# Performance work log

Measured on AMD Instinct MI355X. Metric: run time of the kernel, lower is better.

The kernel has to match this reference:

```python
import jax, jax.numpy as jnp
import numpy as np

T = 4096      # tokens (flattened batch*seq)
DIN = 2048    # input hidden dim
DQ = 2048     # q output dim
DKV = 2048    # per-head-group kv output dim (== DQ here, MHA)
NA = 4        # number of adapters (LoRA/delta models)
R = 16        # lora rank per q/k/v


def setup_inputs() -> dict:
    key = jax.random.key(0)
    ks = jax.random.split(key, 8)
    def rn(k, shape, scale):
        return jax.random.normal(k, shape, dtype=jnp.float32) * scale
    return {
        "x": rn(ks[0], (T, DIN), 1.0),
        "W_base": rn(ks[1], (DQ + 2 * DKV, DIN), DIN ** -0.5),
        "A_buffer_qkv": rn(ks[2], (NA, DIN, 3 * R), DIN ** -0.5),
        "B_buffer_q": rn(ks[3], (NA, R, DQ), R ** -0.5),
        "B_buffer_kv": rn(ks[4], (NA, R, 2 * DKV), R ** -0.5),
        "DeltaW_q": rn(ks[5], (NA, DIN, DQ), DIN ** -0.5),
        "DeltaW_kv": rn(ks[6], (NA, DIN, 2 * DKV), DIN ** -0.5),
        "weight_indices": jax.random.randint(ks[7], (T,), 0, NA, dtype=jnp.int32),
    }


def _ldmm(indices, x, A, B, D):
    """Per-token adapter-indexed (LoRA + dense delta) matmul.
    indices: [T] int, x: [T, din], A: [na, din, r], B: [na, r, dout], D: [na, din, dout].
    out[t] = (x[t] @ A[a]) @ B[a] + x[t] @ D[a]  with a = indices[t].
    Implemented as masked GEMMs over the small fixed adapter set.
    """
    na = A.shape[0]
    out = jnp.zeros((x.shape[0], B.shape[2]), dtype=x.dtype)
    for a in range(na):  # small fixed loop over adapters
        xa = jnp.where((indices == a)[:, None], x, jnp.zeros((), x.dtype))
        out = out + (xa @ A[a]) @ B[a] + xa @ D[a]
    return out


def reference(x, W_base, A_buffer_qkv, B_buffer_q, B_buffer_kv,
              DeltaW_q, DeltaW_kv, weight_indices):
    # base QKV projection (ColumnParallelLinear, no bias): [T, dq + 2*dkv]
    base = x @ W_base.T
    rank = A_buffer_qkv.shape[2] // 3
    b_dim_q = B_buffer_q.shape[2]
    b_dim_kv = B_buffer_kv.shape[2] // 2
    d_dim_kv = DeltaW_kv.shape[2] // 2
    for i in range(3):  # q, k, v slices
        if i == 0:
            o = _ldmm(weight_indices, x,
                      A_buffer_qkv[:, :, :rank], B_buffer_q, DeltaW_q)
            base = base.at[:, :b_dim_q].add(o)
        else:
            o = _ldmm(weight_indices, x,
                      A_buffer_qkv[:, :, i * rank:(i + 1) * rank],
                      B_buffer_kv[:, :, (i - 1) * b_dim_kv:i * b_dim_kv],
                      DeltaW_kv[:, :, (i - 1) * d_dim_kv:i * d_dim_kv])
            base = base.at[:, i * b_dim_kv:(i + 1) * b_dim_kv].add(o)
    return base
```

## Files before the change

kernel.cpp:

```cpp
#include <hip/hip_runtime.h>
#include <stdint.h>

#define T_TOK 4096
#define DIN   2048
#define DQ    2048
#define DKV   2048
#define NOUT  (DQ + 2*DKV)
#define NA    4
#define RLORA 16
#define BM    256
#define BN    256
#define MPAD  (T_TOK + NA*BM)
#define MTILES (MPAD/BM)
#define KX    (DIN + 64)
#define NKT   (KX/32)
#define KSPLIT 16
#define NTBLK (NOUT/BN)
#define NWG   (MTILES*NTBLK)

typedef unsigned short u16;
typedef __attribute__((ext_vector_type(8))) short short8;
typedef __attribute__((ext_vector_type(8))) u16 u16x8;
typedef __attribute__((ext_vector_type(4))) float f32x4;

__device__ __forceinline__ u16 f2bf(float f) {
  uint32_t u = __float_as_uint(f);
  u = (u + 0x7FFFu + ((u >> 16) & 1u)) >> 16;
  return (u16)u;
}
__device__ __forceinline__ float bf2f(u16 u) {
  return __uint_as_float(((uint32_t)u) << 16);
}

typedef __attribute__((address_space(3))) void lds_void;
typedef __attribute__((address_space(1))) void glb_void;

__device__ __forceinline__ void gl_lds16(const void* g, void* l) {
  __builtin_amdgcn_global_load_lds((const glb_void*)(uintptr_t)g,
                                   (lds_void*)(uint32_t)(uintptr_t)l, 16, 0, 0);
}

__global__ void prep_kernel(const int* __restrict__ widx,
                            int* __restrict__ tok,
                            int* __restrict__ tileAdapter) {
  __shared__ int cnt[256][NA];
  __shared__ int total[NA];
  __shared__ int pad_off[NA];
  const int tid = threadIdx.x;
  const int CH = T_TOK / 256;
  const int base = tid * CH;
  int c[NA] = {0, 0, 0, 0};
  for (int i = 0; i < CH; i++) c[widx[base + i]]++;
  for (int a = 0; a < NA; a++) cnt[tid][a] = c[a];
  __syncthreads();
  if (tid < NA) {
    int s = 0;
    for (int i = 0; i < 256; i++) { int v = cnt[i][tid]; cnt[i][tid] = s; s += v; }
    total[tid] = s;
  }
  __syncthreads();
  if (tid == 0) {
    int off = 0;
    for (int a = 0; a < NA; a++) {
      pad_off[a] = off;
      int ntile = (total[a] + BM - 1) / BM;
      for (int tl = 0; tl < ntile; tl++) tileAdapter[off / BM + tl] = a;
      off += ntile * BM;
    }
    for (int tl = off / BM; tl < MTILES; tl++) tileAdapter[tl] = -1;
  }
  __syncthreads();
  for (int i = tid; i < MPAD; i += 256) tok[i] = -1;
  __syncthreads();
  int myoff[NA];
  for (int a = 0; a < NA; a++) myoff[a] = pad_off[a] + cnt[tid][a];
  for (int i = 0; i < CH; i++) {
    int a = widx[base + i];
    tok[myoff[a]++] = base + i;
  }
}

__global__ void gather_kernel(const float* __restrict__ x,
                              const int* __restrict__ tok,
                              u16* __restrict__ Xg) {
  const int row = blockIdx.x;
  const int t = tok[row];
  const int tid = threadIdx.x;
  u16x8* dst = (u16x8*)(Xg + (size_t)row * KX);
  if (t < 0) {
    u16x8 z = {0, 0, 0, 0, 0, 0, 0, 0};
    dst[tid] = z;
    return;
  }
  const f32x4* src = (const f32x4*)(x + (size_t)t * DIN);
  f32x4 v0 = src[tid * 2];
  f32x4 v1 = src[tid * 2 + 1];
  u16x8 o;
  o[0] = f2bf(v0[0]); o[1] = f2bf(v0[1]); o[2] = f2bf(v0[2]); o[3] = f2bf(v0[3]);
  o[4] = f2bf(v1[0]); o[5] = f2bf(v1[1]); o[6] = f2bf(v1[2]); o[7] = f2bf(v1[3]);
  dst[tid] = o;
}

__global__ __launch_bounds__(256) void xa_partial_kernel(
    const u16* __restrict__ Xg, const float* __restrict__ A_qkv,
    const int* __restrict__ tileAdapter, float* __restrict__ Ppart) {
  const int ks = blockIdx.y;
  const int ad = tileAdapter[blockIdx.x >> 1];
  const int a = ad < 0 ? 0 : ad;
  const int kb = ks * (DIN / KSPLIT);
  const int tid = threadIdx.x;
  const int rg = tid >> 2;
  const int jg = tid & 3;
  const int r0 = blockIdx.x * 128 + rg * 2;
  const int j0 = jg * 12;
  __shared__ float ldsA[64][56];
  float acc[2][12];
  #pragma unroll
  for (int r = 0; r < 2; r++)
    #pragma unroll
    for (int j = 0; j < 12; j++) acc[r][j] = 0.f;

  for (int kc = 0; kc < 2; kc++) {
    const int kbase = kb + kc * 64;
    for (int i = tid; i < 64 * 48; i += 256) {
      int kk = i / 48, j = i - kk * 48;
      ldsA[kk][j] = A_qkv[((size_t)a * DIN + kbase + kk) * (3 * RLORA) + j];
    }
    __syncthreads();
    u16x8 xr[2][8];
    #pragma unroll
    for (int r = 0; r < 2; r++)
      #pragma unroll
      for (int q = 0; q < 8; q++)
        xr[r][q] = *(const u16x8*)(Xg + (size_t)(r0 + r) * KX + kbase + q * 8);
    #pragma unroll
    for (int q = 0; q < 8; q++) {
      #pragma unroll
      for (int e = 0; e < 8; e++) {
        const int kk = q * 8 + e;
        f32x4 a0 = *(const f32x4*)&ldsA[kk][j0];
        f32x4 a1 = *(const f32x4*)&ldsA[kk][j0 + 4];
        f32x4 a2 = *(const f32x4*)&ldsA[kk][j0 + 8];
        float x0 = bf2f(xr[0][q][e]);
        float x1 = bf2f(xr[1][q][e]);
        #pragma unroll
        for (int c = 0; c < 4; c++) {
          acc[0][c]     += x0 * a0[c];  acc[1][c]     += x1 * a0[c];
          acc[0][4 + c] += x0 * a1[c];  acc[1][4 + c] += x1 * a1[c];
          acc[0][8 + c] += x0 * a2[c];  acc[1][8 + c] += x1 * a2[c];
        }
      }
    }
    __syncthreads();
  }
  #pragma unroll
  for (int r = 0; r < 2; r++)
    #pragma unroll
    for (int j = 0; j < 12; j++)
      Ppart[((size_t)ks * MPAD + r0 + r) * 48 + j0 + j] = acc[r][j];
}

__global__ void xa_reduce_kernel(const float* __restrict__ Ppart,
                                 u16* __restrict__ Xg) {
  const int gid = blockIdx.x * 256 + threadIdx.x;
  const int row = gid >> 6, j = gid & 63;
  float s = 0.f;
  if (j < 48) {
    #pragma unroll
    for (int sp = 0; sp < KSPLIT; sp++)
      s += Ppart[((size_t)sp * MPAD + row) * 48 + j];
  }
  Xg[(size_t)row * KX + DIN + j] = f2bf(s);
}

__global__ __launch_bounds__(256) void weff2_kernel(
    const float* __restrict__ W_base,
    const float* __restrict__ DW_q, const float* __restrict__ DW_kv,
    u16* __restrict__ Weff) {
  const int k0 = blockIdx.x * 64;
  const int n0 = blockIdx.y * 64;
  const int tid = threadIdx.x;
  const int k8 = (tid & 7) * 8;
  __shared__ float ldsD[64][65];

  f32x4 wb[2][2];
  #pragma unroll
  for (int h = 0; h < 2; h++) {
    const int nn = h * 32 + (tid >> 3);
    const float* p = W_base + (size_t)(n0 + nn) * DIN + k0 + k8;
    wb[h][0] = *(const f32x4*)p;
    wb[h][1] = *(const f32x4*)(p + 4);
  }

  const int ldD  = (n0 < DQ) ? DQ : 2 * DKV;
  const int ncol = (n0 < DQ) ? n0 : n0 - DQ;
  const float* Dbase = (n0 < DQ) ? (DW_q + ncol) : (DW_kv + ncol);
  const size_t Dstride = (n0 < DQ) ? (size_t)DIN * DQ : (size_t)DIN * (2 * DKV);

  const int lkk = tid >> 6;
  const int lnn = tid & 63;

  float v[16];
  {
    const float* Dp = Dbase;
    #pragma unroll
    for (int j = 0; j < 16; j++)
      v[j] = Dp[(size_t)(k0 + lkk + 4 * j) * ldD + lnn];
  }

  for (int a = 0; a < NA; a++) {
    #pragma unroll
    for (int j = 0; j < 16; j++) ldsD[lkk + 4 * j][lnn] = v[j];
    if (a < NA - 1) {
      const float* Dp = Dbase + (size_t)(a + 1) * Dstride;
      #pragma unroll
      for (int j = 0; j < 16; j++)
        v[j] = Dp[(size_t)(k0 + lkk + 4 * j) * ldD + lnn];
    }
    __syncthreads();
    #pragma unroll
    for (int h = 0; h < 2; h++) {
      const int nn = h * 32 + (tid >> 3);
      u16x8 o;
      #pragma unroll
      for (int j = 0; j < 8; j++)
        o[j] = f2bf(wb[h][j >> 2][j & 3] + ldsD[k8 + j][nn]);
      *(u16x8*)(Weff + ((size_t)a * NOUT + n0 + nn) * KX + k0 + k8) = o;
    }
    __syncthreads();
  }
}

__global__ void wslots_kernel(const float* __restrict__ B_q,
                              const float* __restrict__ B_kv,
                              u16* __restrict__ Weff) {
  const int a = blockIdx.y;
  const int n = blockIdx.x * 256 + threadIdx.x;
  const int seg = n >> 11;
  u16 vals[64];
  #pragma unroll
  for (int j = 0; j < 64; j++) vals[j] = 0;
  if (seg == 0) {
    const float* Bp = B_q + ((size_t)a * RLORA) * DQ + n;
    #pragma unroll
    for (int r = 0; r < RLORA; r++) vals[r] = f2bf(Bp[(size_t)r * DQ]);
  } else if (seg == 1) {
    const float* Bp = B_kv + ((size_t)a * RLORA) * (2 * DKV) + (n - DQ);
    #pragma unroll
    for (int r = 0; r < RLORA; r++) vals[RLORA + r] = f2bf(Bp[(size_t)r * (2 * DKV)]);
  } else {
    const float* Bp = B_kv + ((size_t)a * RLORA) * (2 * DKV) + (n - DQ);
    #pragma unroll
    for (int r = 0; r < RLORA; r++) vals[2 * RLORA + r] = f2bf(Bp[(size_t)r * (2 * DKV)]);
  }
  u16* dst = Weff + ((size_t)a * NOUT + n) * KX + DIN;
  #pragma unroll
  for (int v = 0; v < 8; v++) *(u16x8*)(dst + v * 8) = *(u16x8*)(vals + v * 8);
}

#define BAR      asm volatile("s_barrier" ::: "memory")
#define WAITV(n) asm volatile("s_waitcnt vmcnt(" #n ")" ::: "memory")

#define RD_A4(b, mlo) { \
  _Pragma("unroll") for (int q = 0; q < 4; ++q) { \
    const char* rp = ldsc + (b)*16384 + (wm*128 + ((mlo)+q)*16)*64; \
    af[(mlo)+q] = *(const short8*)(rp + laneoff); } }

#define RD_B4(b) { \
  _Pragma("unroll") for (int q = 0; q < 4; ++q) { \
    const char* rp = ldsc + 65536 + (b)*16384 + (wn*64 + q*16)*64; \
    bfr[q] = *(const short8*)(rp + laneoff); } }

#define ST_U01(b, t) { \
  gl_lds16(gAsrc + (size_t)(t)*32, ldsu + (b)*8192 + stid); \
  gl_lds16(gAsrc + (size_t)128*KX + (size_t)(t)*32, ldsu + (b)*8192 + 4096 + stid); }

#define ST_U23(b, t) { \
  gl_lds16(gBsrc + (size_t)(t)*32, ldsu + 32768 + (b)*8192 + stid); \
  gl_lds16(gBsrc + (size_t)128*KX + (size_t)(t)*32, ldsu + 32768 + (b)*8192 + 4096 + stid); }

#define MM4(mlo) { \
  __builtin_amdgcn_s_setprio(1); \
  _Pragma("unroll") for (int mi = 0; mi < 4; ++mi) \
  _Pragma("unroll") for (int ni = 0; ni < 4; ++ni) \
    acc[(mlo)+mi][ni] = __builtin_amdgcn_mfma_f32_16x16x32_bf16( \
        af[(mlo)+mi], bfr[ni], acc[(mlo)+mi][ni], 0, 0, 0); \
  __builtin_amdgcn_s_setprio(0); }

#define TILE(b, t, W) { \
  W; BAR; \
  RD_A4(b, 0); RD_B4(b); ST_U01(((b)+3)&3, (t)+3); \
  BAR; \
  MM4(0); \
  RD_A4(b, 4); ST_U23(((b)+3)&3, (t)+3); \
  BAR; \
  MM4(4); }

#define TILE_N(b, W) { \
  W; BAR; \
  RD_A4(b, 0); RD_B4(b); \
  BAR; \
  MM4(0); \
  RD_A4(b, 4); \
  BAR; \
  MM4(4); }

__global__ __launch_bounds__(512, 2) void gemm256_kernel(
    const u16* __restrict__ Xg, const u16* __restrict__ Weff,
    const int* __restrict__ tok, const int* __restrict__ tileAdapter,
    float* __restrict__ out) {
  __shared__ __align__(16) u16 Lds[65536];

  const int bid = blockIdx.x;
  const int lw = (bid & 7) * (NWG / 8) + (bid >> 3);
  const int pg  = lw / (2 * NTBLK);
  const int rem = lw % (2 * NTBLK);
  const int nt  = rem >> 1;
  const int mt  = pg * 2 + (rem & 1);
  const int a = tileAdapter[mt];
  if (a < 0) return;
  const int m0 = mt * BM, n0 = nt * BN;

  const int tid = threadIdx.x;
  const int l = tid & 63, w = tid >> 6;
  const int wm = w >> 2, wn = w & 3;
  const int fr = l & 15;
  const int laneoff = fr * 64 + ((((l >> 4) ^ ((fr >> 1) & 3))) << 4);

  const int srow = tid >> 2;
  const int scol = (((tid & 3) ^ ((tid >> 3) & 3))) * 8;
  const int stid = tid * 8;
  const u16* gAsrc = Xg + (size_t)(m0 + srow) * KX + scol;
  const u16* gBsrc = Weff + ((size_t)a * NOUT + n0 + srow) * KX + scol;

  u16* ldsu = &Lds[0];
  const char* ldsc = (const char*)ldsu;

  f32x4 acc[8][4];
  #pragma unroll
  for (int i = 0; i < 8; i++)
    #pragma unroll
    for (int j = 0; j < 4; j++) acc[i][j] = (f32x4){0.f, 0.f, 0.f, 0.f};

  short8 af[8], bfr[4];

  ST_U01(0, 0); ST_U23(0, 0);
  ST_U01(1, 1); ST_U23(1, 1);
  ST_U01(2, 2); ST_U23(2, 2);

  for (int p = 0; p < 15; ++p) {
    const int t4 = 4 * p;
    TILE(0, t4 + 0, WAITV(8));
    TILE(1, t4 + 1, WAITV(8));
    TILE(2, t4 + 2, WAITV(8));
    TILE(3, t4 + 3, WAITV(8));
  }
  TILE(0, 60, WAITV(8));
  TILE(1, 61, WAITV(8));
  TILE(2, 62, WAITV(8));
  TILE_N(3, WAITV(8));
  TILE_N(0, WAITV(4));
  TILE_N(1, WAITV(0));

  #pragma unroll
  for (int mi = 0; mi < 8; ++mi) {
    const int rb = m0 + wm * 128 + mi * 16 + ((l >> 4) << 2);
    int tt[4];
    #pragma unroll
    for (int reg = 0; reg < 4; ++reg) tt[reg] = tok[rb + reg];
    #pragma unroll
    for (int ni = 0; ni < 4; ++ni) {
      const int col = n0 + wn * 64 + ni * 16 + fr;
      #pragma unroll
      for (int reg = 0; reg < 4; ++reg)
        if (tt[reg] >= 0) out[(size_t)tt[reg] * NOUT + col] = acc[mi][ni][reg];
    }
  }
}

__global__ void fallback_kernel(const float* __restrict__ x,
                                const float* __restrict__ W_base,
                                const float* __restrict__ A_qkv,
                                const float* __restrict__ B_q,
                                const float* __restrict__ B_kv,
                                const float* __restrict__ DW_q,
                                const float* __restrict__ DW_kv,
                                const int* __restrict__ widx,
                                float* __restrict__ out) {
  const int t = blockIdx.x;
  const int n = blockIdx.y * 256 + threadIdx.x;
  const int a = widx[t];
  __shared__ float xs[DIN];
  __shared__ float ys[3 * RLORA];
  for (int k = threadIdx.x; k < DIN; k += 256) xs[k] = x[(size_t)t * DIN + k];
  __syncthreads();
  if (threadIdx.x < 3 * RLORA) {
    float s = 0.f;
    const float* Ap = A_qkv + (size_t)a * DIN * (3 * RLORA) + threadIdx.x;
    for (int k = 0; k < DIN; k++) s += xs[k] * Ap[(size_t)k * (3 * RLORA)];
    ys[threadIdx.x] = s;
  }
  __syncthreads();
  const float* dcol; int ldD, roff; const float* bcol; int ldB;
  if (n < DQ) {
    dcol = DW_q + (size_t)a * DIN * DQ + n; ldD = DQ; roff = 0;
    bcol = B_q + (size_t)a * RLORA * DQ + n; ldB = DQ;
  } else {
    dcol = DW_kv + (size_t)a * DIN * (2 * DKV) + (n - DQ); ldD = 2 * DKV;
    roff = (n < 2 * DQ) ? RLORA : 2 * RLORA;
    bcol = B_kv + (size_t)a * RLORA * (2 * DKV) + (n - DQ); ldB = 2 * DKV;
  }
  const float* wrow = W_base + (size_t)n * DIN;
  float acc = 0.f;
  for (int k = 0; k < DIN; k++) acc += xs[k] * (wrow[k] + dcol[(size_t)k * ldD]);
  for (int r = 0; r < RLORA; r++) acc += ys[roff + r] * bcol[(size_t)r * ldB];
  out[(size_t)t * NOUT + n] = acc;
}

extern "C" void kernel_launch(void* const* d_in, const int* in_sizes, int n_in,
                              void* d_out, int out_size, void* d_ws, size_t ws_size,
                              hipStream_t stream) {
  const float* x      = (const float*)d_in[0];
  const float* W_base = (const float*)d_in[1];
  const float* A_qkv  = (const float*)d_in[2];
  const float* B_q    = (const float*)d_in[3];
  const float* B_kv   = (const float*)d_in[4];
  const float* DW_q   = (const float*)d_in[5];
  const float* DW_kv  = (const float*)d_in[6];
  const int*   widx   = (const int*)d_in[7];
  float* out = (float*)d_out;

  const size_t WEFF_BYTES = (size_t)NA * NOUT * KX * sizeof(u16);
  const size_t XG_BYTES   = (size_t)MPAD * KX * sizeof(u16);
  const size_t TOK_BYTES  = (size_t)MPAD * sizeof(int);
  const size_t TILE_BYTES = (size_t)MTILES * sizeof(int);
  const size_t need = WEFF_BYTES + XG_BYTES + TOK_BYTES + TILE_BYTES;

  if (ws_size < need) {
    fallback_kernel<<<dim3(T_TOK, NOUT / 256), 256, 0, stream>>>(
        x, W_base, A_qkv, B_q, B_kv, DW_q, DW_kv, widx, out);
    return;
  }

  char* ws = (char*)d_ws;
  u16* Weff = (u16*)ws;
  u16* Xg   = (u16*)(ws + WEFF_BYTES);
  int* tok  = (int*)(ws + WEFF_BYTES + XG_BYTES);
  int* tileAdapter = tok + MPAD;
  float* Ppart = (float*)ws;

  prep_kernel<<<1, 256, 0, stream>>>(widx, tok, tileAdapter);
  gather_kernel<<<MPAD, 256, 0, stream>>>(x, tok, Xg);
  xa_partial_kernel<<<dim3(MPAD / 128, KSPLIT), 256, 0, stream>>>(
      Xg, A_qkv, tileAdapter, Ppart);
  xa_reduce_kernel<<<MPAD * 64 / 256, 256, 0, stream>>>(Ppart, Xg);
  weff2_kernel<<<dim3(DIN / 64, NOUT / 64), 256, 0, stream>>>(
      W_base, DW_q, DW_kv, Weff);
  wslots_kernel<<<dim3(NOUT / 256, NA), 256, 0, stream>>>(B_q, B_kv, Weff);
  gemm256_kernel<<<dim3(NWG), 512, 0, stream>>>(
      Xg, Weff, tok, tileAdapter, out);
}
```

Before: 257.4 us.

## Switch main GEMM to 4-wave workgroups with 128x128 per-wave tiles

The 256x256 GEMM tile moves from 8 waves (128x64 per wave) to 4 waves (128x128 per wave, 8x8 MFMA accumulators), launched with 256 threads and launch bounds of 1 block. The split LDS-read/MFMA phases with three barriers per k-step become one barrier per step, with all fragments read up front and then 64 MFMAs issued. The intent is more MFMA work per LDS fragment loaded and less barrier overhead. The cost is much higher register pressure (256 accumulator VGPRs), which risks spills, lower occupancy and less latency hiding.

```diff
diff --git a/kernel.cpp b/kernel.cpp
--- a/kernel.cpp
+++ b/kernel.cpp
@@ -261,51 +261,31 @@
 #define BAR      asm volatile("s_barrier" ::: "memory")
 #define WAITV(n) asm volatile("s_waitcnt vmcnt(" #n ")" ::: "memory")
 
-#define RD_A4(b, mlo) { \
-  _Pragma("unroll") for (int q = 0; q < 4; ++q) { \
-    const char* rp = ldsc + (b)*16384 + (wm*128 + ((mlo)+q)*16)*64; \
-    af[(mlo)+q] = *(const short8*)(rp + laneoff); } }
-
-#define RD_B4(b) { \
-  _Pragma("unroll") for (int q = 0; q < 4; ++q) { \
-    const char* rp = ldsc + 65536 + (b)*16384 + (wn*64 + q*16)*64; \
-    bfr[q] = *(const short8*)(rp + laneoff); } }
-
-#define ST_U01(b, t) { \
-  gl_lds16(gAsrc + (size_t)(t)*32, ldsu + (b)*8192 + stid); \
-  gl_lds16(gAsrc + (size_t)128*KX + (size_t)(t)*32, ldsu + (b)*8192 + 4096 + stid); }
-
-#define ST_U23(b, t) { \
-  gl_lds16(gBsrc + (size_t)(t)*32, ldsu + 32768 + (b)*8192 + stid); \
-  gl_lds16(gBsrc + (size_t)128*KX + (size_t)(t)*32, ldsu + 32768 + (b)*8192 + 4096 + stid); }
-
-#define MM4(mlo) { \
+#define ST(b, t) { \
+  _Pragma("unroll") for (int j = 0; j < 4; ++j) { \
+    gl_lds16(gAsrc + (size_t)(j * 64) * KX + (size_t)(t) * 32, \
+             ldsu + (b)*8192 + j*2048 + tid*8); \
+    gl_lds16(gBsrc + (size_t)(j * 64) * KX + (size_t)(t) * 32, \
+             ldsu + 32768 + (b)*8192 + j*2048 + tid*8); } }
+
+#define RD(b) { \
+  _Pragma("unroll") for (int q = 0; q < 8; ++q) \
+    af[q] = *(const short8*)(ldsc + (b)*16384 + (wm*128 + q*16)*64 + laneoff); \
+  _Pragma("unroll") for (int q = 0; q < 8; ++q) \
+    bf[q] = *(const short8*)(ldsc + 65536 + (b)*16384 + (wn*128 + q*16)*64 + laneoff); }
+
+#define MM64 { \
   __builtin_amdgcn_s_setprio(1); \
-  _Pragma("unroll") for (int mi = 0; mi < 4; ++mi) \
-  _Pragma("unroll") for (int ni = 0; ni < 4; ++ni) \
-    acc[(mlo)+mi][ni] = __builtin_amdgcn_mfma_f32_16x16x32_bf16( \
-        af[(mlo)+mi], bfr[ni], acc[(mlo)+mi][ni], 0, 0, 0); \
+  _Pragma("unroll") for (int q = 0; q < 8; ++q) \
+  _Pragma("unroll") for (int r = 0; r < 8; ++r) \
+    acc[q][r] = __builtin_amdgcn_mfma_f32_16x16x32_bf16( \
+        af[q], bf[r], acc[q][r], 0, 0, 0); \
   __builtin_amdgcn_s_setprio(0); }
 
-#define TILE(b, t, W) { \
-  W; BAR; \
-  RD_A4(b, 0); RD_B4(b); ST_U01(((b)+3)&3, (t)+3); \
-  BAR; \
-  MM4(0); \
-  RD_A4(b, 4); ST_U23(((b)+3)&3, (t)+3); \
-  BAR; \
-  MM4(4); }
-
-#define TILE_N(b, W) { \
-  W; BAR; \
-  RD_A4(b, 0); RD_B4(b); \
-  BAR; \
-  MM4(0); \
-  RD_A4(b, 4); \
-  BAR; \
-  MM4(4); }
-
-__global__ __launch_bounds__(512, 2) void gemm256_kernel(
+#define TILE_S(b, t) { WAITV(16); BAR; RD(b); ST(((b)+3)&3, (t)+3); MM64; }
+#define TILE_N(b, W) { W; BAR; RD(b); MM64; }
+
+__global__ __launch_bounds__(256, 1) void gemm4w_kernel(
     const u16* __restrict__ Xg, const u16* __restrict__ Weff,
     const int* __restrict__ tok, const int* __restrict__ tileAdapter,
     float* __restrict__ out) {
@@ -323,43 +303,40 @@
 
   const int tid = threadIdx.x;
   const int l = tid & 63, w = tid >> 6;
-  const int wm = w >> 2, wn = w & 3;
+  const int wm = w >> 1, wn = w & 1;
   const int fr = l & 15;
   const int laneoff = fr * 64 + ((((l >> 4) ^ ((fr >> 1) & 3))) << 4);
 
   const int srow = tid >> 2;
   const int scol = (((tid & 3) ^ ((tid >> 3) & 3))) * 8;
-  const int stid = tid * 8;
   const u16* gAsrc = Xg + (size_t)(m0 + srow) * KX + scol;
   const u16* gBsrc = Weff + ((size_t)a * NOUT + n0 + srow) * KX + scol;
 
   u16* ldsu = &Lds[0];
   const char* ldsc = (const char*)ldsu;
 
-  f32x4 acc[8][4];
+  f32x4 acc[8][8];
   #pragma unroll
   for (int i = 0; i < 8; i++)
     #pragma unroll
-    for (int j = 0; j < 4; j++) acc[i][j] = (f32x4){0.f, 0.f, 0.f, 0.f};
-
-  short8 af[8], bfr[4];
-
-  ST_U01(0, 0); ST_U23(0, 0);
-  ST_U01(1, 1); ST_U23(1, 1);
-  ST_U01(2, 2); ST_U23(2, 2);
+    for (int j = 0; j < 8; j++) acc[i][j] = (f32x4){0.f, 0.f, 0.f, 0.f};
+
+  short8 af[8], bf[8];
+
+  ST(0, 0); ST(1, 1); ST(2, 2);
 
   for (int p = 0; p < 15; ++p) {
     const int t4 = 4 * p;
-    TILE(0, t4 + 0, WAITV(8));
-    TILE(1, t4 + 1, WAITV(8));
-    TILE(2, t4 + 2, WAITV(8));
-    TILE(3, t4 + 3, WAITV(8));
-  }
-  TILE(0, 60, WAITV(8));
-  TILE(1, 61, WAITV(8));
-  TILE(2, 62, WAITV(8));
-  TILE_N(3, WAITV(8));
-  TILE_N(0, WAITV(4));
+    TILE_S(0, t4 + 0);
+    TILE_S(1, t4 + 1);
+    TILE_S(2, t4 + 2);
+    TILE_S(3, t4 + 3);
+  }
+  TILE_S(0, 60);
+  TILE_S(1, 61);
+  TILE_S(2, 62);
+  TILE_N(3, WAITV(16));
+  TILE_N(0, WAITV(8));
   TILE_N(1, WAITV(0));
 
   #pragma unroll
@@ -369,8 +346,8 @@
     #pragma unroll
     for (int reg = 0; reg < 4; ++reg) tt[reg] = tok[rb + reg];
     #pragma unroll
-    for (int ni = 0; ni < 4; ++ni) {
-      const int col = n0 + wn * 64 + ni * 16 + fr;
+    for (int ni = 0; ni < 8; ++ni) {
+      const int col = n0 + wn * 128 + ni * 16 + fr;
       #pragma unroll
       for (int reg = 0; reg < 4; ++reg)
         if (tt[reg] >= 0) out[(size_t)tt[reg] * NOUT + col] = acc[mi][ni][reg];
@@ -457,6 +434,6 @@
   weff2_kernel<<<dim3(DIN / 64, NOUT / 64), 256, 0, stream>>>(
       W_base, DW_q, DW_kv, Weff);
   wslots_kernel<<<dim3(NOUT / 256, NA), 256, 0, stream>>>(B_q, B_kv, Weff);
-  gemm256_kernel<<<dim3(NWG), 512, 0, stream>>>(
+  gemm4w_kernel<<<dim3(NWG), 256, 0, stream>>>(
       Xg, Weff, tok, tileAdapter, out);
 }
```

Measured after the change: 279.3 us. 8.5% more time.
